# Performance work log

Hardware: AMD Instinct MI355X
Metric: run time of the kernel (lower is better)

The kernel has to match this reference:

```python
import jax, jax.numpy as jnp
import numpy as np

N, E, G = 50000, 800000, 500
F_IN, H_DIM, L, NH, HD, OUT = 74, 256, 4, 8, 32, 1
SLOPE, EPS = 0.2, 1e-5


def setup_inputs() -> dict:
    key = jax.random.key(0)
    ks = jax.random.split(key, 24)
    rn = lambda k, s, sc: jax.random.normal(k, s, jnp.float32) * sc
    inp = {
        "x": jax.random.normal(ks[0], (N, F_IN), jnp.float32),
        "edge_index": jax.random.randint(ks[1], (2, E), 0, N),
        "batch": jnp.sort(jax.random.randint(ks[2], (N,), 0, G)),
        "in_w": rn(ks[3], (F_IN, H_DIM), 1.0 / np.sqrt(F_IN)),
        "in_b": jnp.zeros((H_DIM,), jnp.float32),
        "wl": rn(ks[4], (L, H_DIM, H_DIM), 1.0 / np.sqrt(H_DIM)),
        "wl_b": jnp.zeros((L, H_DIM), jnp.float32),
        "wr": rn(ks[5], (L, H_DIM, H_DIM), 1.0 / np.sqrt(H_DIM)),
        "wr_b": jnp.zeros((L, H_DIM), jnp.float32),
        "att": rn(ks[6], (L, NH, HD), 1.0 / np.sqrt(HD)),
        "gat_b": jnp.zeros((L, H_DIM), jnp.float32),
        "ln_g": jnp.ones((L, H_DIM), jnp.float32),
        "ln_b": jnp.zeros((L, H_DIM), jnp.float32),
        "out_w": rn(ks[7], (H_DIM, H_DIM), 1.0 / np.sqrt(H_DIM)),
        "out_b": jnp.zeros((H_DIM,), jnp.float32),
        "p1_w": rn(ks[8], (H_DIM, H_DIM // 2), 1.0 / np.sqrt(H_DIM)),
        "p1_b": jnp.zeros((H_DIM // 2,), jnp.float32),
        "bn1_g": jnp.ones((H_DIM // 2,), jnp.float32),
        "bn1_b": jnp.zeros((H_DIM // 2,), jnp.float32),
        "p2_w": rn(ks[9], (H_DIM // 2, H_DIM // 4), 1.0 / np.sqrt(H_DIM // 2)),
        "p2_b": jnp.zeros((H_DIM // 4,), jnp.float32),
        "bn2_g": jnp.ones((H_DIM // 4,), jnp.float32),
        "bn2_b": jnp.zeros((H_DIM // 4,), jnp.float32),
        "p3_w": rn(ks[10], (H_DIM // 4, OUT), 1.0 / np.sqrt(H_DIM // 4)),
        "p3_b": jnp.zeros((OUT,), jnp.float32),
    }
    return inp


def _layer_norm(x, g, b):
    m = x.mean(-1, keepdims=True)
    v = ((x - m) ** 2).mean(-1, keepdims=True)
    return (x - m) * jax.lax.rsqrt(v + EPS) * g + b


def _batch_norm(x, g, b):
    m = x.mean(0)
    v = ((x - m) ** 2).mean(0)
    return (x - m) * jax.lax.rsqrt(v + EPS) * g + b


def _gatv2(h, src, dst, wl, wl_b, wr, wr_b, att, bias, n):
    xl = (h @ wl + wl_b).reshape(n, NH, HD)  # source transform
    xr = (h @ wr + wr_b).reshape(n, NH, HD)  # target transform
    e = jax.nn.leaky_relu(xl[src] + xr[dst], SLOPE)      # [E, H, D]
    score = jnp.einsum('ehd,hd->eh', e, att)             # [E, H]
    smax = jax.ops.segment_max(score, dst, num_segments=n)
    num = jnp.exp(score - smax[dst])
    den = jax.ops.segment_sum(num, dst, num_segments=n)
    alpha = num / (den[dst] + 1e-16)                     # segment softmax per dst
    out = jax.ops.segment_sum(xl[src] * alpha[:, :, None], dst, num_segments=n)
    return out.reshape(n, NH * HD) + bias


def reference(x, edge_index, batch, in_w, in_b, wl, wl_b, wr, wr_b, att, gat_b,
              ln_g, ln_b, out_w, out_b, p1_w, p1_b, bn1_g, bn1_b,
              p2_w, p2_b, bn2_g, bn2_b, p3_w, p3_b):
    n = x.shape[0]
    loops = jnp.arange(n)
    src = jnp.concatenate([edge_index[0], loops])  # add self-loops (PyG default)
    dst = jnp.concatenate([edge_index[1], loops])
    h = x @ in_w + in_b
    for i in range(L):
        res = h
        g = _gatv2(h, src, dst, wl[i], wl_b[i], wr[i], wr_b[i], att[i], gat_b[i], n)
        if i > 0:
            g = g + res
        h = jax.nn.relu(_layer_norm(g, ln_g[i], ln_b[i]))
    h = h @ out_w + out_b
    cnt = jax.ops.segment_sum(jnp.ones((n,), h.dtype), batch, num_segments=G)
    gr = jax.ops.segment_sum(h, batch, num_segments=G) / jnp.maximum(cnt, 1.0)[:, None]
    z = jax.nn.relu(_batch_norm(gr @ p1_w + p1_b, bn1_g, bn1_b))
    z = jax.nn.relu(_batch_norm(z @ p2_w + p2_b, bn2_g, bn2_b))
    return z @ p3_w + p3_b
```

## Files before the change

### kernel.cpp

```cpp
#include <hip/hip_runtime.h>
#include <hip/hip_bf16.h>

#define F_IN   74
#define KPAD   96
#define HDIM   256
#define NHEAD  8
#define HEADD  32
#define NLAYER 4
#define SLOPE  0.2f
#define EPSN   1e-5f

typedef __attribute__((ext_vector_type(8))) short bf16x8;
typedef __attribute__((ext_vector_type(4))) float f32x4;
typedef __attribute__((ext_vector_type(2))) float f32x2;

__device__ __forceinline__ float bf2f(unsigned short u){
  union { unsigned int i; float f; } x; x.i = ((unsigned int)u) << 16; return x.f;
}
__device__ __forceinline__ unsigned short f2bf(float f){
  union { float f; unsigned int i; } x; x.f = f;
  unsigned int u = x.i;
  return (unsigned short)((u + 0x7FFFu + ((u >> 16) & 1u)) >> 16);
}
__device__ __forceinline__ f32x2 bfpair(unsigned int u){
  union { unsigned int i; float f; } lo, hi;
  lo.i = u << 16; hi.i = u & 0xffff0000u;
  return (f32x2){lo.f, hi.f};
}
__device__ __forceinline__ float dpp_sum8(float p){
  int t;
  t = __builtin_amdgcn_update_dpp(0, __float_as_int(p), 0xB1, 0xF, 0xF, true);
  p += __int_as_float(t);
  t = __builtin_amdgcn_update_dpp(0, __float_as_int(p), 0x4E, 0xF, 0xF, true);
  p += __int_as_float(t);
  t = __builtin_amdgcn_update_dpp(0, __float_as_int(p), 0x141, 0xF, 0xF, true);
  p += __int_as_float(t);
  return p;
}

#define GLOAD16(g, s) __builtin_amdgcn_global_load_lds( \
  (const __attribute__((address_space(1))) void*)(g), \
  (__attribute__((address_space(3))) void*)(s), 16, 0, 0)

__global__ void k_hist(const int* __restrict__ dst, int* __restrict__ deg, int e){
  int i = blockIdx.x * 256 + threadIdx.x;
  if (i < e) atomicAdd(&deg[dst[i]], 1);
}

__global__ __launch_bounds__(256) void k_scan1(const int* __restrict__ deg,
    int* __restrict__ rowp, int* __restrict__ bsum, int n){
  __shared__ int wsum[4];
  const int tid = threadIdx.x, lane = tid & 63, wid = tid >> 6;
  const int i = blockIdx.x * 256 + tid;
  int v = (i < n) ? (deg[i] + 1) : 0;
  int xv = v;
  #pragma unroll
  for (int off = 1; off < 64; off <<= 1){
    int t = __shfl_up(xv, off);
    if (lane >= off) xv += t;
  }
  if (lane == 63) wsum[wid] = xv;
  __syncthreads();
  int woff = 0, total = 0;
  #pragma unroll
  for (int w = 0; w < 4; ++w){
    int s = wsum[w];
    total += s;
    if (w < wid) woff += s;
  }
  if (i < n) rowp[i] = woff + xv - v;
  if (tid == 0) bsum[blockIdx.x] = total;
}
__global__ __launch_bounds__(256) void k_scan2(const int* __restrict__ bsum,
    int* __restrict__ boff, int nb){
  __shared__ int wsum[4];
  const int tid = threadIdx.x, lane = tid & 63, wid = tid >> 6;
  int v = (tid < nb) ? bsum[tid] : 0;
  int xv = v;
  #pragma unroll
  for (int off = 1; off < 64; off <<= 1){
    int t = __shfl_up(xv, off);
    if (lane >= off) xv += t;
  }
  if (lane == 63) wsum[wid] = xv;
  __syncthreads();
  int woff = 0, total = 0;
  #pragma unroll
  for (int w = 0; w < 4; ++w){
    int s = wsum[w];
    total += s;
    if (w < wid) woff += s;
  }
  if (tid <= nb) boff[tid] = woff + xv - v;
  if (tid == 0) boff[nb] = total;
}
__global__ void k_scan3(int* __restrict__ rowp, int* __restrict__ cur,
                        const int* __restrict__ boff, int n, int nb){
  int i = blockIdx.x * 256 + threadIdx.x;
  if (i < n){
    int v = rowp[i] + boff[blockIdx.x];
    rowp[i] = v;
    cur[i] = v;
  }
  if (i == 0) rowp[n] = boff[nb];
}

__global__ void k_fill2(const int* __restrict__ src, const int* __restrict__ dst,
                        int* __restrict__ cur, unsigned int* __restrict__ csr,
                        int e, int n){
  int i = blockIdx.x * 256 + threadIdx.x;
  if (i < e){
    int p = atomicAdd(&cur[dst[i]], 1);
    csr[p] = ((unsigned int)src[i]) << 10;
  } else if (i < e + n){
    int v = i - e;
    int p = atomicAdd(&cur[v], 1);
    csr[p] = ((unsigned int)v) << 10;
  }
}

__global__ __launch_bounds__(256) void k_prep(
    const float* __restrict__ wl, const float* __restrict__ wr,
    const float* __restrict__ out_w, const float* __restrict__ in_w,
    const float* __restrict__ wl_b, const float* __restrict__ wr_b,
    const float* __restrict__ x,
    unsigned short* __restrict__ WtLR, unsigned short* __restrict__ WtO,
    unsigned short* __restrict__ WtI, float* __restrict__ bconc,
    unsigned short* __restrict__ xb, int n)
{
  const int b = blockIdx.x;
  const int tid = threadIdx.x;
  if (b < 576){
    __shared__ float tile[32][33];
    const float* Wm;
    unsigned short* Wo;
    int rem;
    if (b < 512){
      const int matset = b >> 8;
      const int mat = (b >> 6) & 3;
      rem = b & 63;
      const float* srcw = matset ? wr : wl;
      Wm = srcw + (size_t)mat * HDIM * HDIM;
      Wo = WtLR + (size_t)mat * 512 * HDIM + (matset ? (size_t)256 * HDIM : 0);
    } else {
      rem = b - 512;
      Wm = out_w; Wo = WtO;
    }
    const int c0 = (rem & 7) * 32, r0 = (rem >> 3) * 32;
    const int tx = tid & 31, ty = tid >> 5;
    #pragma unroll
    for (int i = 0; i < 32; i += 8)
      tile[ty + i][tx] = Wm[(size_t)(r0 + ty + i) * HDIM + c0 + tx];
    __syncthreads();
    #pragma unroll
    for (int i = 0; i < 32; i += 8)
      Wo[(size_t)(c0 + ty + i) * HDIM + r0 + tx] = f2bf(tile[tx][ty + i]);
  } else if (b < 672){
    int idx = (b - 576) * 256 + tid;
    int c = idx / KPAD, k = idx - c * KPAD;
    float v = (k < F_IN) ? in_w[(size_t)k * HDIM + c] : 0.f;
    WtI[idx] = f2bf(v);
  } else if (b < 680){
    int i = (b - 672) * 256 + tid;
    if (i < NLAYER * 512){
      int layer = i >> 9, c = i & 511;
      bconc[i] = (c < 256) ? wl_b[layer * 256 + c] : wr_b[layer * 256 + (c - 256)];
    }
  } else {
    int idx = (b - 680) * 256 + tid;
    if (idx < n * KPAD){
      int row = idx / KPAD, k = idx - row * KPAD;
      float v = (k < F_IN) ? x[(size_t)row * F_IN + k] : 0.f;
      xb[idx] = f2bf(v);
    }
  }
}

__global__ __launch_bounds__(256) void k_inproj_mfma(
    const unsigned short* __restrict__ xb, const unsigned short* __restrict__ Wt,
    const float* __restrict__ bias, unsigned short* __restrict__ C, int M)
{
  const int l = threadIdx.x & 63;
  const int w = threadIdx.x >> 6;
  const int wm = w >> 1, wn = w & 1;
  const int row0 = blockIdx.x * 128;
  const int col0 = blockIdx.y * 128;

  f32x4 acc[4][4];
  #pragma unroll
  for (int i = 0; i < 4; ++i)
    #pragma unroll
    for (int j = 0; j < 4; ++j) acc[i][j] = (f32x4){0.f, 0.f, 0.f, 0.f};

  #pragma unroll
  for (int kk = 0; kk < 3; ++kk){
    const int kof = kk * 32 + (l >> 4) * 8;
    bf16x8 af[4], bfr[4];
    #pragma unroll
    for (int mi = 0; mi < 4; ++mi){
      int row = row0 + wm * 64 + mi * 16 + (l & 15);
      if (row > M - 1) row = M - 1;
      af[mi] = *(const bf16x8*)(xb + (size_t)row * KPAD + kof);
    }
    #pragma unroll
    for (int ni = 0; ni < 4; ++ni){
      const int col = col0 + wn * 64 + ni * 16 + (l & 15);
      bfr[ni] = *(const bf16x8*)(Wt + (size_t)col * KPAD + kof);
    }
    #pragma unroll
    for (int mi = 0; mi < 4; ++mi)
      #pragma unroll
      for (int ni = 0; ni < 4; ++ni)
        acc[mi][ni] = __builtin_amdgcn_mfma_f32_16x16x32_bf16(
            af[mi], bfr[ni], acc[mi][ni], 0, 0, 0);
  }

  #pragma unroll
  for (int mi = 0; mi < 4; ++mi){
    #pragma unroll
    for (int ni = 0; ni < 4; ++ni){
      const int col = col0 + wn * 64 + ni * 16 + (l & 15);
      const float bv = bias[col];
      #pragma unroll
      for (int r = 0; r < 4; ++r){
        const int row = row0 + wm * 64 + mi * 16 + (l >> 4) * 4 + r;
        if (row < M) C[(size_t)row * HDIM + col] = f2bf(acc[mi][ni][r] + bv);
      }
    }
  }
}

__global__ __launch_bounds__(256) void k_gemm_mfma(
    const unsigned short* __restrict__ A, const unsigned short* __restrict__ Wt,
    const float* __restrict__ bias, unsigned short* __restrict__ C, int M, int ldc)
{
  __shared__ unsigned short As[2][128 * 64];
  __shared__ unsigned short Bs[2][128 * 64];
  const int tid = threadIdx.x;
  const int l   = tid & 63;
  const int w   = tid >> 6;
  const int wm  = w >> 1, wn = w & 1;
  const int row0 = blockIdx.x * 128;
  const int col0 = blockIdx.y * 128;

  const int srow   = l >> 3;
  const int schunk = l & 7;

  f32x4 acc[4][4];
  #pragma unroll
  for (int i = 0; i < 4; ++i)
    #pragma unroll
    for (int j = 0; j < 4; ++j) acc[i][j] = (f32x4){0.f, 0.f, 0.f, 0.f};

  auto stage = [&](int buf, int k0){
    #pragma unroll
    for (int i = 0; i < 4; ++i){
      const int rloc = w * 32 + i * 8 + srow;
      const int sw   = (schunk ^ (rloc & 7)) * 16;
      int ra = row0 + rloc; if (ra > M - 1) ra = M - 1;
      const char* srcA = (const char*)(A + (size_t)ra * HDIM + k0) + sw;
      GLOAD16(srcA, &As[buf][(w * 32 + i * 8) * 64]);
      const char* srcB = (const char*)(Wt + (size_t)(col0 + rloc) * HDIM + k0) + sw;
      GLOAD16(srcB, &Bs[buf][(w * 32 + i * 8) * 64]);
    }
  };

  auto compute = [&](int buf){
    #pragma unroll
    for (int kk = 0; kk < 2; ++kk){
      bf16x8 af[4], bfr[4];
      #pragma unroll
      for (int mi = 0; mi < 4; ++mi){
        const int row = wm * 64 + mi * 16 + (l & 15);
        const int t   = (kk * 4 + (l >> 4)) ^ (row & 7);
        af[mi] = *(const bf16x8*)((const char*)&As[buf][0] + row * 128 + t * 16);
      }
      #pragma unroll
      for (int ni = 0; ni < 4; ++ni){
        const int nn = wn * 64 + ni * 16 + (l & 15);
        const int t  = (kk * 4 + (l >> 4)) ^ (nn & 7);
        bfr[ni] = *(const bf16x8*)((const char*)&Bs[buf][0] + nn * 128 + t * 16);
      }
      #pragma unroll
      for (int mi = 0; mi < 4; ++mi)
        #pragma unroll
        for (int ni = 0; ni < 4; ++ni)
          acc[mi][ni] = __builtin_amdgcn_mfma_f32_16x16x32_bf16(
              af[mi], bfr[ni], acc[mi][ni], 0, 0, 0);
    }
  };

  stage(0, 0);
  int cur = 0;
  #pragma unroll
  for (int t = 0; t < 4; ++t){
    if (t < 3){
      stage(cur ^ 1, (t + 1) * 64);
      asm volatile("s_waitcnt vmcnt(8)" ::: "memory");
    } else {
      asm volatile("s_waitcnt vmcnt(0)" ::: "memory");
    }
    __builtin_amdgcn_s_barrier();
    compute(cur);
    asm volatile("" ::: "memory");
    __builtin_amdgcn_s_barrier();
    cur ^= 1;
  }

  #pragma unroll
  for (int mi = 0; mi < 4; ++mi){
    #pragma unroll
    for (int ni = 0; ni < 4; ++ni){
      const int col = col0 + wn * 64 + ni * 16 + (l & 15);
      const float bv = bias[col];
      #pragma unroll
      for (int r = 0; r < 4; ++r){
        const int row = row0 + wm * 64 + mi * 16 + (l >> 4) * 4 + r;
        if (row < M) C[(size_t)row * ldc + col] = f2bf(acc[mi][ni][r] + bv);
      }
    }
  }
}

__global__ __launch_bounds__(256) void k_gat(
    const unsigned short* __restrict__ xlr,
    const int* __restrict__ rp, const unsigned int* __restrict__ csr,
    const float* __restrict__ att, const float* __restrict__ gb,
    const float* __restrict__ lg, const float* __restrict__ lb,
    const unsigned short* __restrict__ hold, unsigned short* __restrict__ hnew,
    int n, int use_res)
{
  const int node = blockIdx.x * 4 + (threadIdx.x >> 6);
  if (node >= n) return;
  const int lane = threadIdx.x & 63;
  const int elem = lane << 2;
  const int head = lane >> 3;
  float4 attv = *(const float4*)(att + head * HEADD + (elem & 31));
  const f32x2 av01 = {attv.x, attv.y}, av23 = {attv.z, attv.w};
  uint2 ur = *(const uint2*)(xlr + (size_t)node * 512 + 256 + elem);
  const f32x2 r01 = bfpair(ur.x), r23 = bfpair(ur.y);

  const char* xbase = (const char*)xlr + (elem << 1);

  f32x2 a01 = {0.f, 0.f}, a23 = {0.f, 0.f};
  float l = 0.f;

  auto edgeq = [&](uint2 uu, f32x2& x01, f32x2& x23)->float{
    x01 = bfpair(uu.x); x23 = bfpair(uu.y);
    f32x2 t01 = x01 + r01, t23 = x23 + r23;
    f32x2 m01 = __builtin_elementwise_max(t01, t01 * SLOPE);
    f32x2 m23 = __builtin_elementwise_max(t23, t23 * SLOPE);
    f32x2 d = m01 * av01 + m23 * av23;
    float p = dpp_sum8(d.x + d.y);
    return __expf(p);
  };

  const int e0 = rp[node], e1 = rp[node + 1];
  int e = e0;
  for (; e + 4 <= e1; e += 4){
    unsigned int o0 = csr[e], o1 = csr[e + 1], o2 = csr[e + 2], o3 = csr[e + 3];
    uint2 u0 = *(const uint2*)(xbase + o0);
    uint2 u1 = *(const uint2*)(xbase + o1);
    uint2 u2 = *(const uint2*)(xbase + o2);
    uint2 u3 = *(const uint2*)(xbase + o3);
    f32x2 x01, x23;
    float q0 = edgeq(u0, x01, x23);
    a01 += q0 * x01; a23 += q0 * x23;
    float q1 = edgeq(u1, x01, x23);
    a01 += q1 * x01; a23 += q1 * x23;
    float q2 = edgeq(u2, x01, x23);
    a01 += q2 * x01; a23 += q2 * x23;
    float q3 = edgeq(u3, x01, x23);
    a01 += q3 * x01; a23 += q3 * x23;
    l += (q0 + q1) + (q2 + q3);
  }
  for (; e < e1; ++e){
    unsigned int o = csr[e];
    uint2 u = *(const uint2*)(xbase + o);
    f32x2 x01, x23;
    float q = edgeq(u, x01, x23);
    l += q;
    a01 += q * x01; a23 += q * x23;
  }

  const float inv = 1.f / l;
  const size_t base = (size_t)node * HDIM + elem;
  float f0 = a01.x * inv + gb[elem + 0];
  float f1 = a01.y * inv + gb[elem + 1];
  float f2 = a23.x * inv + gb[elem + 2];
  float f3 = a23.y * inv + gb[elem + 3];
  if (use_res){
    ushort4 hv = *(const ushort4*)(hold + base);
    f0 += bf2f(hv.x); f1 += bf2f(hv.y); f2 += bf2f(hv.z); f3 += bf2f(hv.w);
  }
  float s = f0 + f1 + f2 + f3;
  #pragma unroll
  for (int off = 1; off < 64; off <<= 1) s += __shfl_xor(s, off);
  const float mean = s * (1.f / HDIM);
  float d0 = f0 - mean, d1 = f1 - mean, d2 = f2 - mean, d3 = f3 - mean;
  float q = d0 * d0 + d1 * d1 + d2 * d2 + d3 * d3;
  #pragma unroll
  for (int off = 1; off < 64; off <<= 1) q += __shfl_xor(q, off);
  const float rs = rsqrtf(q * (1.f / HDIM) + EPSN);
  float o0 = d0 * rs * lg[elem + 0] + lb[elem + 0]; o0 = o0 > 0.f ? o0 : 0.f;
  float o1 = d1 * rs * lg[elem + 1] + lb[elem + 1]; o1 = o1 > 0.f ? o1 : 0.f;
  float o2 = d2 * rs * lg[elem + 2] + lb[elem + 2]; o2 = o2 > 0.f ? o2 : 0.f;
  float o3 = d3 * rs * lg[elem + 3] + lb[elem + 3]; o3 = o3 > 0.f ? o3 : 0.f;
  ushort4 st; st.x = f2bf(o0); st.y = f2bf(o1); st.z = f2bf(o2); st.w = f2bf(o3);
  *(ushort4*)(hnew + base) = st;
}

__global__ __launch_bounds__(256) void k_pool2(
    const unsigned short* __restrict__ ho, const int* __restrict__ batch,
    float* __restrict__ gr, int n)
{
  const int g = blockIdx.x;
  int lo = 0, hi = n;
  while (lo < hi){ int mid = (lo + hi) >> 1; if (batch[mid] < g) lo = mid + 1; else hi = mid; }
  const int s = lo;
  hi = n;
  while (lo < hi){ int mid = (lo + hi) >> 1; if (batch[mid] < g + 1) lo = mid + 1; else hi = mid; }
  const int e = lo;
  const int j = threadIdx.x;
  float acc = 0.f;
  for (int i = s; i < e; ++i) acc += bf2f(ho[(size_t)i * HDIM + j]);
  int c = e - s; if (c < 1) c = 1;
  gr[(size_t)g * HDIM + j] = acc / (float)c;
}

__global__ void k_fc(const float* __restrict__ in, const float* __restrict__ w,
                     const float* __restrict__ b, float* __restrict__ out,
                     int kin, int kout){
  __shared__ float s[256];
  int g = blockIdx.x, j = threadIdx.x;
  for (int k = j; k < kin; k += blockDim.x) s[k] = in[(size_t)g * kin + k];
  __syncthreads();
  float a = b[j];
  for (int k = 0; k < kin; ++k) a = fmaf(s[k], w[k * kout + j], a);
  out[(size_t)g * kout + j] = a;
}

__global__ __launch_bounds__(256) void k_bn(float* __restrict__ z,
    const float* __restrict__ gam, const float* __restrict__ bet, int g_, int c_){
  const int c = blockIdx.x;
  float s = 0.f, s2 = 0.f;
  for (int r = threadIdx.x; r < g_; r += 256){
    float v = z[(size_t)r * c_ + c];
    s += v; s2 += v * v;
  }
  #pragma unroll
  for (int off = 1; off < 64; off <<= 1){ s += __shfl_xor(s, off); s2 += __shfl_xor(s2, off); }
  __shared__ float sw[4], sw2[4];
  __shared__ float smean, srstd;
  int lane = threadIdx.x & 63, wid = threadIdx.x >> 6;
  if (lane == 0){ sw[wid] = s; sw2[wid] = s2; }
  __syncthreads();
  if (threadIdx.x == 0){
    float ts = sw[0] + sw[1] + sw[2] + sw[3];
    float ts2 = sw2[0] + sw2[1] + sw2[2] + sw2[3];
    float mm = ts / g_;
    float vv = ts2 / g_ - mm * mm;
    smean = mm; srstd = rsqrtf(vv + EPSN);
  }
  __syncthreads();
  const float mm = smean, rs = srstd, gg = gam[c], bb = bet[c];
  for (int r = threadIdx.x; r < g_; r += 256){
    float v = (z[(size_t)r * c_ + c] - mm) * rs * gg + bb;
    z[(size_t)r * c_ + c] = v > 0.f ? v : 0.f;
  }
}

__global__ __launch_bounds__(256) void k_out(const float* __restrict__ z,
    const float* __restrict__ w, const float* __restrict__ b,
    float* __restrict__ out, int g_){
  int g = blockIdx.x * 4 + (threadIdx.x >> 6);
  if (g >= g_) return;
  int lane = threadIdx.x & 63;
  float v = z[(size_t)g * 64 + lane] * w[lane];
  #pragma unroll
  for (int off = 1; off < 64; off <<= 1) v += __shfl_xor(v, off);
  if (lane == 0) out[g] = v + b[0];
}

extern "C" void kernel_launch(void* const* d_in, const int* in_sizes, int n_in,
                              void* d_out, int out_size, void* d_ws, size_t ws_size,
                              hipStream_t stream)
{
  const float* x     = (const float*)d_in[0];
  const int*   ei    = (const int*)  d_in[1];
  const int*   batch = (const int*)  d_in[2];
  const float* in_w  = (const float*)d_in[3];
  const float* in_b  = (const float*)d_in[4];
  const float* wl    = (const float*)d_in[5];
  const float* wl_b  = (const float*)d_in[6];
  const float* wr    = (const float*)d_in[7];
  const float* wr_b  = (const float*)d_in[8];
  const float* att   = (const float*)d_in[9];
  const float* gat_b = (const float*)d_in[10];
  const float* ln_g  = (const float*)d_in[11];
  const float* ln_b  = (const float*)d_in[12];
  const float* out_w = (const float*)d_in[13];
  const float* out_b = (const float*)d_in[14];
  const float* p1_w  = (const float*)d_in[15];
  const float* p1_b  = (const float*)d_in[16];
  const float* bn1_g = (const float*)d_in[17];
  const float* bn1_b = (const float*)d_in[18];
  const float* p2_w  = (const float*)d_in[19];
  const float* p2_b  = (const float*)d_in[20];
  const float* bn2_g = (const float*)d_in[21];
  const float* bn2_b = (const float*)d_in[22];
  const float* p3_w  = (const float*)d_in[23];
  const float* p3_b  = (const float*)d_in[24];

  const int n = in_sizes[0] / F_IN;
  const int e = in_sizes[1] / 2;
  const int g = out_size;
  const int nb = (n + 255) / 256;

  char* p = (char*)d_ws;
  auto take = [&](size_t bytes)->char*{
    char* q = p; p += ((bytes + 255) & ~(size_t)255); return q;
  };
  unsigned short* hA   = (unsigned short*)take((size_t)n * HDIM * 2);
  unsigned short* hB   = (unsigned short*)take((size_t)n * HDIM * 2);
  unsigned short* xlr  = (unsigned short*)take((size_t)n * 512 * 2);
  unsigned short* WtLR = (unsigned short*)take((size_t)NLAYER * 512 * HDIM * 2);
  unsigned short* WtO  = (unsigned short*)take((size_t)HDIM * HDIM * 2);
  unsigned short* WtI  = (unsigned short*)take((size_t)HDIM * KPAD * 2);
  float* bconc = (float*)take((size_t)NLAYER * 512 * 4);
  int*   deg   = (int*)take((size_t)n * 4);
  int*   rowp  = (int*)take((size_t)(n + 1) * 4);
  int*   cur   = (int*)take((size_t)n * 4);
  unsigned int* csr = (unsigned int*)take((size_t)(e + n) * 4);
  int*   bsum  = (int*)take((size_t)(nb + 1) * 4);
  int*   boff  = (int*)take((size_t)(nb + 1) * 4);
  float* gr    = (float*)take((size_t)g * HDIM * 4);
  float* z1    = (float*)take((size_t)g * 128 * 4);
  float* z2    = (float*)take((size_t)g * 64 * 4);
  unsigned short* xb = xlr;
  (void)ws_size; (void)n_in;

  hipMemsetAsync(deg, 0, (size_t)n * 4, stream);
  k_hist<<<(e + 255) / 256, 256, 0, stream>>>(ei + e, deg, e);
  k_scan1<<<nb, 256, 0, stream>>>(deg, rowp, bsum, n);
  k_scan2<<<1, 256, 0, stream>>>(bsum, boff, nb);
  k_scan3<<<nb, 256, 0, stream>>>(rowp, cur, boff, n, nb);
  k_fill2<<<(e + n + 255) / 256, 256, 0, stream>>>(ei, ei + e, cur, csr, e, n);

  const int xconv_blocks = (n * KPAD + 255) / 256;
  k_prep<<<680 + xconv_blocks, 256, 0, stream>>>(
      wl, wr, out_w, in_w, wl_b, wr_b, x, WtLR, WtO, WtI, bconc, xb, n);

  k_inproj_mfma<<<dim3((n + 127) / 128, 2), 256, 0, stream>>>(xb, WtI, in_b, hA, n);

  unsigned short* hcur = hA;
  unsigned short* hnext = hB;
  for (int i = 0; i < NLAYER; ++i){
    k_gemm_mfma<<<dim3((n + 127) / 128, 4), 256, 0, stream>>>(
        hcur, WtLR + (size_t)i * 512 * HDIM, bconc + i * 512, xlr, n, 512);
    k_gat<<<(n + 3) / 4, 256, 0, stream>>>(xlr, rowp, csr,
        att + (size_t)i * NHEAD * HEADD, gat_b + i * HDIM,
        ln_g + i * HDIM, ln_b + i * HDIM, hcur, hnext, n, i > 0 ? 1 : 0);
    unsigned short* t = hcur; hcur = hnext; hnext = t;
  }
  k_gemm_mfma<<<dim3((n + 127) / 128, 2), 256, 0, stream>>>(
      hcur, WtO, out_b, hnext, n, HDIM);

  k_pool2<<<g, 256, 0, stream>>>(hnext, batch, gr, n);

  k_fc<<<g, 128, 0, stream>>>(gr, p1_w, p1_b, z1, HDIM, 128);
  k_bn<<<128, 256, 0, stream>>>(z1, bn1_g, bn1_b, g, 128);
  k_fc<<<g, 64, 0, stream>>>(z1, p2_w, p2_b, z2, 128, 64);
  k_bn<<<64, 256, 0, stream>>>(z2, bn2_g, bn2_b, g, 64);
  k_out<<<(g + 3) / 4, 256, 0, stream>>>(z2, p3_w, p3_b, (float*)d_out, g);
}
```

Baseline: 682.0 us.

## Pre-swizzle GEMM weights into MFMA fragment layout, unroll GAT edges, use exp2 and DPP reductions

Weights are now stored during prep in an MFMA-fragment-ordered layout, so the GEMM loads B fragments straight from global memory into registers and drops the LDS B buffers and some barriers. The GAT kernel folds log2(e) into the attention vector so it can use exp2f, unrolls the edge loop to 8 gathers in flight, and replaces the shuffle-based LayerNorm reductions with DPP row sums plus two shuffles. The goal is less LDS traffic and synchronisation in the GEMM and more memory-level parallelism and fewer cross-lane ops in GAT. The risk is that B reads are repeated per wave from global/L2 instead of shared through LDS, and the wider unroll raises register pressure.

```diff
diff --git a/kernel.cpp b/kernel.cpp
--- a/kernel.cpp
+++ b/kernel.cpp
@@ -9,6 +9,7 @@
 #define NLAYER 4
 #define SLOPE  0.2f
 #define EPSN   1e-5f
+#define LOG2E  1.44269504088896f
 
 typedef __attribute__((ext_vector_type(8))) short bf16x8;
 typedef __attribute__((ext_vector_type(4))) float f32x4;
@@ -34,6 +35,13 @@
   t = __builtin_amdgcn_update_dpp(0, __float_as_int(p), 0x4E, 0xF, 0xF, true);
   p += __int_as_float(t);
   t = __builtin_amdgcn_update_dpp(0, __float_as_int(p), 0x141, 0xF, 0xF, true);
+  p += __int_as_float(t);
+  return p;
+}
+__device__ __forceinline__ float dpp_sum16(float p){
+  int t;
+  p = dpp_sum8(p);
+  t = __builtin_amdgcn_update_dpp(0, __float_as_int(p), 0x140, 0xF, 0xF, true);
   p += __int_as_float(t);
   return p;
 }
@@ -134,17 +142,18 @@
     __shared__ float tile[32][33];
     const float* Wm;
     unsigned short* Wo;
-    int rem;
+    int rem, colbase;
     if (b < 512){
       const int matset = b >> 8;
       const int mat = (b >> 6) & 3;
       rem = b & 63;
       const float* srcw = matset ? wr : wl;
       Wm = srcw + (size_t)mat * HDIM * HDIM;
-      Wo = WtLR + (size_t)mat * 512 * HDIM + (matset ? (size_t)256 * HDIM : 0);
+      Wo = WtLR + (size_t)mat * 512 * HDIM;
+      colbase = matset * 256;
     } else {
       rem = b - 512;
-      Wm = out_w; Wo = WtO;
+      Wm = out_w; Wo = WtO; colbase = 0;
     }
     const int c0 = (rem & 7) * 32, r0 = (rem >> 3) * 32;
     const int tx = tid & 31, ty = tid >> 5;
@@ -153,8 +162,13 @@
       tile[ty + i][tx] = Wm[(size_t)(r0 + ty + i) * HDIM + c0 + tx];
     __syncthreads();
     #pragma unroll
-    for (int i = 0; i < 32; i += 8)
-      Wo[(size_t)(c0 + ty + i) * HDIM + r0 + tx] = f2bf(tile[tx][ty + i]);
+    for (int i = 0; i < 32; i += 8){
+      const int col = colbase + c0 + ty + i;
+      const int k   = r0 + tx;
+      const int cb = col >> 4, ks = k >> 5;
+      const int lf = (col & 15) | (((k >> 3) & 3) << 4);
+      Wo[((size_t)(cb * 8 + ks) * 64 + lf) * 8 + (k & 7)] = f2bf(tile[tx][ty + i]);
+    }
   } else if (b < 672){
     int idx = (b - 576) * 256 + tid;
     int c = idx / KPAD, k = idx - c * KPAD;
@@ -235,7 +249,6 @@
     const float* __restrict__ bias, unsigned short* __restrict__ C, int M, int ldc)
 {
   __shared__ unsigned short As[2][128 * 64];
-  __shared__ unsigned short Bs[2][128 * 64];
   const int tid = threadIdx.x;
   const int l   = tid & 63;
   const int w   = tid >> 6;
@@ -252,7 +265,7 @@
     #pragma unroll
     for (int j = 0; j < 4; ++j) acc[i][j] = (f32x4){0.f, 0.f, 0.f, 0.f};
 
-  auto stage = [&](int buf, int k0){
+  auto stageA = [&](int buf, int k0){
     #pragma unroll
     for (int i = 0; i < 4; ++i){
       const int rloc = w * 32 + i * 8 + srow;
@@ -260,51 +273,45 @@
       int ra = row0 + rloc; if (ra > M - 1) ra = M - 1;
       const char* srcA = (const char*)(A + (size_t)ra * HDIM + k0) + sw;
       GLOAD16(srcA, &As[buf][(w * 32 + i * 8) * 64]);
-      const char* srcB = (const char*)(Wt + (size_t)(col0 + rloc) * HDIM + k0) + sw;
-      GLOAD16(srcB, &Bs[buf][(w * 32 + i * 8) * 64]);
     }
   };
 
-  auto compute = [&](int buf){
+  const unsigned short* Bf = Wt + ((size_t)(col0 / 16 + wn * 4) * 8 * 64 + l) * 8;
+
+  stageA(0, 0);
+  asm volatile("s_waitcnt vmcnt(0)" ::: "memory");
+  __builtin_amdgcn_s_barrier();
+  int buf = 0;
+  #pragma unroll
+  for (int t = 0; t < 4; ++t){
+    bf16x8 bfr[2][4];
+    #pragma unroll
+    for (int kk = 0; kk < 2; ++kk)
+      #pragma unroll
+      for (int ni = 0; ni < 4; ++ni)
+        bfr[kk][ni] = *(const bf16x8*)(Bf + ((size_t)ni * 8 + (t * 2 + kk)) * 64 * 8);
+    if (t < 3) stageA(buf ^ 1, (t + 1) * 64);
     #pragma unroll
     for (int kk = 0; kk < 2; ++kk){
-      bf16x8 af[4], bfr[4];
+      bf16x8 af[4];
       #pragma unroll
       for (int mi = 0; mi < 4; ++mi){
         const int row = wm * 64 + mi * 16 + (l & 15);
-        const int t   = (kk * 4 + (l >> 4)) ^ (row & 7);
-        af[mi] = *(const bf16x8*)((const char*)&As[buf][0] + row * 128 + t * 16);
-      }
-      #pragma unroll
-      for (int ni = 0; ni < 4; ++ni){
-        const int nn = wn * 64 + ni * 16 + (l & 15);
-        const int t  = (kk * 4 + (l >> 4)) ^ (nn & 7);
-        bfr[ni] = *(const bf16x8*)((const char*)&Bs[buf][0] + nn * 128 + t * 16);
+        const int tt  = (kk * 4 + (l >> 4)) ^ (row & 7);
+        af[mi] = *(const bf16x8*)((const char*)&As[buf][0] + row * 128 + tt * 16);
       }
       #pragma unroll
       for (int mi = 0; mi < 4; ++mi)
         #pragma unroll
         for (int ni = 0; ni < 4; ++ni)
           acc[mi][ni] = __builtin_amdgcn_mfma_f32_16x16x32_bf16(
-              af[mi], bfr[ni], acc[mi][ni], 0, 0, 0);
-    }
-  };
-
-  stage(0, 0);
-  int cur = 0;
-  #pragma unroll
-  for (int t = 0; t < 4; ++t){
+              af[mi], bfr[kk][ni], acc[mi][ni], 0, 0, 0);
+    }
     if (t < 3){
-      stage(cur ^ 1, (t + 1) * 64);
-      asm volatile("s_waitcnt vmcnt(8)" ::: "memory");
-    } else {
       asm volatile("s_waitcnt vmcnt(0)" ::: "memory");
-    }
-    __builtin_amdgcn_s_barrier();
-    compute(cur);
-    asm volatile("" ::: "memory");
-    __builtin_amdgcn_s_barrier();
-    cur ^= 1;
+      __builtin_amdgcn_s_barrier();
+      buf ^= 1;
+    }
   }
 
   #pragma unroll
@@ -336,7 +343,8 @@
   const int elem = lane << 2;
   const int head = lane >> 3;
   float4 attv = *(const float4*)(att + head * HEADD + (elem & 31));
-  const f32x2 av01 = {attv.x, attv.y}, av23 = {attv.z, attv.w};
+  const f32x2 av01 = {attv.x * LOG2E, attv.y * LOG2E};
+  const f32x2 av23 = {attv.z * LOG2E, attv.w * LOG2E};
   uint2 ur = *(const uint2*)(xlr + (size_t)node * 512 + 256 + elem);
   const f32x2 r01 = bfpair(ur.x), r23 = bfpair(ur.y);
 
@@ -352,27 +360,27 @@
     f32x2 m23 = __builtin_elementwise_max(t23, t23 * SLOPE);
     f32x2 d = m01 * av01 + m23 * av23;
     float p = dpp_sum8(d.x + d.y);
-    return __expf(p);
+    return exp2f(p);
   };
 
   const int e0 = rp[node], e1 = rp[node + 1];
   int e = e0;
-  for (; e + 4 <= e1; e += 4){
-    unsigned int o0 = csr[e], o1 = csr[e + 1], o2 = csr[e + 2], o3 = csr[e + 3];
-    uint2 u0 = *(const uint2*)(xbase + o0);
-    uint2 u1 = *(const uint2*)(xbase + o1);
-    uint2 u2 = *(const uint2*)(xbase + o2);
-    uint2 u3 = *(const uint2*)(xbase + o3);
-    f32x2 x01, x23;
-    float q0 = edgeq(u0, x01, x23);
-    a01 += q0 * x01; a23 += q0 * x23;
-    float q1 = edgeq(u1, x01, x23);
-    a01 += q1 * x01; a23 += q1 * x23;
-    float q2 = edgeq(u2, x01, x23);
-    a01 += q2 * x01; a23 += q2 * x23;
-    float q3 = edgeq(u3, x01, x23);
-    a01 += q3 * x01; a23 += q3 * x23;
-    l += (q0 + q1) + (q2 + q3);
+  for (; e + 8 <= e1; e += 8){
+    unsigned int off[8];
+    #pragma unroll
+    for (int j = 0; j < 8; ++j) off[j] = csr[e + j];
+    uint2 u[8];
+    #pragma unroll
+    for (int j = 0; j < 8; ++j) u[j] = *(const uint2*)(xbase + off[j]);
+    float lacc = 0.f;
+    #pragma unroll
+    for (int j = 0; j < 8; ++j){
+      f32x2 x01, x23;
+      float q = edgeq(u[j], x01, x23);
+      lacc += q;
+      a01 += q * x01; a23 += q * x23;
+    }
+    l += lacc;
   }
   for (; e < e1; ++e){
     unsigned int o = csr[e];
@@ -394,13 +402,15 @@
     f0 += bf2f(hv.x); f1 += bf2f(hv.y); f2 += bf2f(hv.z); f3 += bf2f(hv.w);
   }
   float s = f0 + f1 + f2 + f3;
-  #pragma unroll
-  for (int off = 1; off < 64; off <<= 1) s += __shfl_xor(s, off);
+  s = dpp_sum16(s);
+  s += __shfl_xor(s, 16);
+  s += __shfl_xor(s, 32);
   const float mean = s * (1.f / HDIM);
   float d0 = f0 - mean, d1 = f1 - mean, d2 = f2 - mean, d3 = f3 - mean;
   float q = d0 * d0 + d1 * d1 + d2 * d2 + d3 * d3;
-  #pragma unroll
-  for (int off = 1; off < 64; off <<= 1) q += __shfl_xor(q, off);
+  q = dpp_sum16(q);
+  q += __shfl_xor(q, 16);
+  q += __shfl_xor(q, 32);
   const float rs = rsqrtf(q * (1.f / HDIM) + EPSN);
   float o0 = d0 * rs * lg[elem + 0] + lb[elem + 0]; o0 = o0 > 0.f ? o0 : 0.f;
   float o1 = d1 * rs * lg[elem + 1] + lb[elem + 1]; o1 = o1 > 0.f ? o1 : 0.f;
```

After: 721.2 us. 1.06x slower.
